# Performance work log

Measured on AMD Instinct MI355X. Metric: run time of the kernel, lower is better.

The kernel has to match this reference:

```python
import jax, jax.numpy as jnp
import numpy as np

B, LQ, LK = 16, 256, 256
DQ = DK = DV = H = 256


def setup_inputs() -> dict:
    key = jax.random.key(0)
    ks = jax.random.split(key, 7)
    queries = jax.random.normal(ks[0], (B, LQ, DQ), dtype=jnp.float32)
    keys = jax.random.normal(ks[1], (B, LK, DK), dtype=jnp.float32)
    values = jax.random.normal(ks[2], (B, LK, DV), dtype=jnp.float32)
    valid_lens = jax.random.randint(ks[3], (B,), 1, LK + 1).astype(jnp.int32)
    W_q = jax.random.normal(ks[4], (DQ, H), dtype=jnp.float32) / np.sqrt(DQ)
    W_k = jax.random.normal(ks[5], (DK, H), dtype=jnp.float32) / np.sqrt(DK)
    w_v = jax.random.normal(ks[6], (H,), dtype=jnp.float32) / np.sqrt(H)
    return {"queries": queries, "keys": keys, "values": values,
            "valid_lens": valid_lens, "W_q": W_q, "W_k": W_k, "w_v": w_v}


def reference(queries, keys, values, valid_lens, W_q, W_k, w_v):
    # Project queries and keys to the hidden size (no bias)
    q = jnp.einsum('bqd,dh->bqh', queries, W_q)          # (B, Lq, H)
    k = jnp.einsum('bkd,dh->bkh', keys, W_k)             # (B, Lk, H)
    # Broadcast-add, tanh, then contract with w_v -> scores (B, Lq, Lk)
    features = jnp.tanh(q[:, :, None, :] + k[:, None, :, :])  # (B, Lq, Lk, H)
    scores = jnp.einsum('bqkh,h->bqk', features, w_v)
    # Masked softmax over last axis: positions >= valid_len get -1e6
    mask = jnp.arange(scores.shape[-1]) < valid_lens[:, None, None]  # (B,1,Lk) bcast
    scores = jnp.where(mask, scores, jnp.float32(-1e6))
    attn = jax.nn.softmax(scores, axis=-1)
    # Dropout is identity at inference (training=False)
    return jnp.einsum('bqk,bkv->bqv', attn, values)      # (B, Lq, Dv)
```

## Files before the change

### kernel.cpp

```cpp
#include <hip/hip_runtime.h>

using bf16x8 = __attribute__((ext_vector_type(8))) __bf16;
using f32x4  = __attribute__((ext_vector_type(4))) float;
using f32x2  = __attribute__((ext_vector_type(2))) float;
using us8    = __attribute__((ext_vector_type(8))) unsigned short;

#define TWO_LOG2E 2.8853900817779268f
#define LOG2E 1.4426950408889634f

__device__ __forceinline__ unsigned short f2bf(float x) {
  unsigned int u = __float_as_uint(x);
  u = (u + 0x7fffu + ((u >> 16) & 1u)) >> 16;
  return (unsigned short)u;
}
__device__ __forceinline__ float bf2f(unsigned short h) {
  return __uint_as_float(((unsigned int)h) << 16);
}
__device__ __forceinline__ f32x2 pk_fma(f32x2 a, f32x2 b, f32x2 c) {
  return __builtin_elementwise_fma(a, b, c);
}

__global__ __launch_bounds__(256) void tcast_kernel(
    const float* __restrict__ Wq, const float* __restrict__ Wk,
    const float* __restrict__ vals, const float* __restrict__ wv,
    const int* __restrict__ vlens,
    unsigned short* __restrict__ wt_hi, unsigned short* __restrict__ wt_lo,
    unsigned short* __restrict__ vt_hi, unsigned short* __restrict__ vt_lo,
    float* __restrict__ wv2, float* __restrict__ Wsum,
    int* __restrict__ ctr, int* __restrict__ cum) {
  if (blockIdx.x == 0) {
    int t = threadIdx.x;
    wv2[t] = -2.0f * wv[t];
    if (t < 64) {
      float s = wv[t] + wv[t + 64] + wv[t + 128] + wv[t + 192];
#pragma unroll
      for (int off = 1; off < 64; off <<= 1) s += __shfl_xor(s, off, 64);
      if (t == 0) Wsum[0] = s;
    }
    if (t == 0) {
      ctr[0] = 0;
      int c = 0;
      for (int b = 0; b < 16; ++b) {
        cum[b] = c;
        c += ((vlens[b] + 31) >> 5) << 3;
      }
      cum[16] = c;
    }
  }
  __shared__ float tile[32][33];
  int m = blockIdx.x >> 6;
  int ts = blockIdx.x & 63;
  int R0 = (ts >> 3) << 5, C0 = (ts & 7) << 5;
  const float* src = (m == 0) ? Wq : (m == 1) ? Wk : (vals + ((m - 2) << 16));
  int r = threadIdx.x >> 3, c4 = (threadIdx.x & 7) << 2;
  float4 v = *(const float4*)(src + (R0 + r) * 256 + C0 + c4);
  tile[r][c4] = v.x; tile[r][c4 + 1] = v.y; tile[r][c4 + 2] = v.z; tile[r][c4 + 3] = v.w;
  __syncthreads();
  float o0 = tile[c4 + 0][r], o1 = tile[c4 + 1][r];
  float o2 = tile[c4 + 2][r], o3 = tile[c4 + 3][r];
  unsigned short h0 = f2bf(o0), h1 = f2bf(o1), h2 = f2bf(o2), h3 = f2bf(o3);
  int base = ((m < 2) ? (m << 16) : ((m - 2) << 16)) + (C0 + r) * 256 + R0 + c4;
  unsigned short* dh = (m < 2) ? wt_hi : vt_hi;
  unsigned short* dl = (m < 2) ? wt_lo : vt_lo;
  *(ushort4*)(dh + base) = make_ushort4(h0, h1, h2, h3);
  *(ushort4*)(dl + base) = make_ushort4(f2bf(o0 - bf2f(h0)), f2bf(o1 - bf2f(h1)),
                                        f2bf(o2 - bf2f(h2)), f2bf(o3 - bf2f(h3)));
}

__global__ __launch_bounds__(256, 4) void proj_kernel(
    const float* __restrict__ q, const float* __restrict__ kk,
    const unsigned short* __restrict__ w_hi, const unsigned short* __restrict__ w_lo,
    const int* __restrict__ vlens, float* __restrict__ Rq, float* __restrict__ RkT) {
  int wave = threadIdx.x >> 6, lane = threadIdx.x & 63;
  int mt = (blockIdx.x << 1) + (wave & 1);
  int m0 = mt << 4;
  int g = mt >> 8;
  if (g) {
    int bb = (m0 >> 8) & 15;
    if ((m0 & 255) >= vlens[bb]) return;
  }
  int r = lane & 15, qd = lane >> 4;
  int row = m0 + r;
  const float* A = (g == 0) ? (q + row * 256) : (kk + (row - 4096) * 256);
  bf16x8 ah[8], al[8];
#pragma unroll
  for (int s = 0; s < 8; ++s) {
    const float* p = A + qd * 8 + s * 32;
    float4 f0 = *(const float4*)p;
    float4 f1 = *(const float4*)(p + 4);
    float fv[8] = {f0.x, f0.y, f0.z, f0.w, f1.x, f1.y, f1.z, f1.w};
#pragma unroll
    for (int j = 0; j < 8; ++j) {
      __bf16 h = (__bf16)fv[j];
      ah[s][j] = h;
      al[s][j] = (__bf16)(fv[j] - (float)h);
    }
  }
  int nbase = (blockIdx.y << 6) + ((wave >> 1) << 5);
#pragma unroll
  for (int tI = 0; tI < 2; ++tI) {
    int n0 = nbase + (tI << 4);
    int boff = (g << 16) + (n0 + r) * 256 + qd * 8;
    f32x4 acc = {0.f, 0.f, 0.f, 0.f};
#pragma unroll
    for (int s = 0; s < 8; ++s) {
      bf16x8 bh = *(const bf16x8*)(w_hi + boff + s * 32);
      bf16x8 bl = *(const bf16x8*)(w_lo + boff + s * 32);
      acc = __builtin_amdgcn_mfma_f32_16x16x32_bf16(ah[s], bh, acc, 0, 0, 0);
      acc = __builtin_amdgcn_mfma_f32_16x16x32_bf16(ah[s], bl, acc, 0, 0, 0);
      acc = __builtin_amdgcn_mfma_f32_16x16x32_bf16(al[s], bh, acc, 0, 0, 0);
    }
    f32x4 ex;
#pragma unroll
    for (int i = 0; i < 4; ++i) {
      float l = acc[i] * TWO_LOG2E;
      l = fminf(fmaxf(l, -27.f), 27.f);
      ex[i] = __builtin_amdgcn_exp2f(l);
    }
    if (g == 0) {
#pragma unroll
      for (int i = 0; i < 4; ++i)
        Rq[(m0 + qd * 4 + i) * 256 + n0 + r] = ex[i];
    } else {
      int b = (m0 >> 8) & 15;
      int kloc = (m0 & 255) + qd * 4;
      *(f32x4*)(RkT + (b << 16) + (n0 + r) * 256 + kloc) = ex;
    }
  }
}

__global__ __launch_bounds__(256, 8) void scores_kernel(
    const float* __restrict__ Rq, const float* __restrict__ RkT,
    const float* __restrict__ wv2, const float* __restrict__ Wsum,
    const int* __restrict__ cum, int* __restrict__ ctr,
    float* __restrict__ sc) {
  __shared__ __align__(16) float rqs[32 * 76];
  __shared__ __align__(16) float kT[64 * 34];
  __shared__ int s_item;
  const int t = threadIdx.x;
  const int tq = t >> 4, tk = t & 15;
  const int sr = t >> 3, shb = (t & 7) << 3;
  const int hrow = t >> 2, kq = (t & 3) << 3;
  const int total = cum[16];
  const float ws = Wsum[0];

  for (;;) {
    __syncthreads();
    if (t == 0) s_item = atomicAdd(ctr, 1);
    __syncthreads();
    const int w = s_item;
    if (w >= total) return;
    int b = 0;
    while (cum[b + 1] <= w) ++b;
    const int local = w - cum[b];
    const int k0 = (local >> 3) << 5;
    const int q0 = (local & 7) << 5;
    const int qrow = (b << 8) + q0;
    f32x2 a0 = {0.f, 0.f}, a1 = {0.f, 0.f};

    for (int hc = 0; hc < 4; ++hc) {
      if (hc) __syncthreads();
      const float* gq = Rq + (qrow + sr) * 256 + (hc << 6) + shb;
      *(float4*)(rqs + sr * 76 + shb)     = *(const float4*)gq;
      *(float4*)(rqs + sr * 76 + shb + 4) = *(const float4*)(gq + 4);
      const float* gk = RkT + (b << 16) + ((hc << 6) + hrow) * 256 + k0 + kq;
      *(float4*)(kT + hrow * 34 + kq)     = *(const float4*)gk;
      *(float4*)(kT + hrow * 34 + kq + 4) = *(const float4*)(gk + 4);
      __syncthreads();
#pragma unroll 2
      for (int h = 0; h < 64; h += 4) {
        f32x4 qa = *(const f32x4*)(rqs + tq * 76 + h);
        f32x4 qb = *(const f32x4*)(rqs + (tq + 16) * 76 + h);
        f32x4 wm = *(const f32x4*)(wv2 + (hc << 6) + h);
#pragma unroll
        for (int j = 0; j < 4; ++j) {
          f32x2 rk = *(const f32x2*)(kT + (h + j) * 34 + (tk << 1));
          f32x2 wj = (f32x2)(wm[j]);
          f32x2 d0 = pk_fma(rk, (f32x2)(qa[j]), (f32x2)(1.0f));
          f32x2 d1 = pk_fma(rk, (f32x2)(qb[j]), (f32x2)(1.0f));
          f32x2 r0, r1;
          r0.x = __uint_as_float(0x7EF311C3u - __float_as_uint(d0.x));
          r0.y = __uint_as_float(0x7EF311C3u - __float_as_uint(d0.y));
          r1.x = __uint_as_float(0x7EF311C3u - __float_as_uint(d1.x));
          r1.y = __uint_as_float(0x7EF311C3u - __float_as_uint(d1.y));
          r0 = r0 * pk_fma(-d0, r0, (f32x2)(2.0f));
          r1 = r1 * pk_fma(-d1, r1, (f32x2)(2.0f));
          a0 = pk_fma(r0, wj, a0);
          a1 = pk_fma(r1, wj, a1);
        }
      }
    }
    a0 += (f32x2)(ws);
    a1 += (f32x2)(ws);
    *(f32x2*)(sc + ((qrow + tq) << 8) + k0 + (tk << 1)) = a0;
    *(f32x2*)(sc + ((qrow + tq + 16) << 8) + k0 + (tk << 1)) = a1;
  }
}

__global__ __launch_bounds__(256) void av_fused_kernel(
    const float* __restrict__ sc, const int* __restrict__ vlens,
    const unsigned short* __restrict__ vhi, const unsigned short* __restrict__ vlo,
    float* __restrict__ out) {
  __shared__ __align__(16) unsigned short athi[16 * 264];
  const int wave = threadIdx.x >> 6, lane = threadIdx.x & 63;
  const int b = blockIdx.x;
  const int nh = blockIdx.y;
  const int m0 = blockIdx.z << 4;
  const int vl = vlens[b];

  {
    int row = (wave << 2) + (lane & 3);
    int c0 = (lane >> 2) << 4;
    const float* srow = sc + ((b << 8) + m0 + row) * 256 + c0;
    float4 x0 = *(const float4*)(srow);
    float4 x1 = *(const float4*)(srow + 4);
    float4 x2 = *(const float4*)(srow + 8);
    float4 x3 = *(const float4*)(srow + 12);
    float p[16] = {x0.x, x0.y, x0.z, x0.w, x1.x, x1.y, x1.z, x1.w,
                   x2.x, x2.y, x2.z, x2.w, x3.x, x3.y, x3.z, x3.w};
#pragma unroll
    for (int i = 0; i < 16; ++i)
      if (c0 + i >= vl) p[i] = -1e6f;
    float mx = p[0];
#pragma unroll
    for (int i = 1; i < 16; ++i) mx = fmaxf(mx, p[i]);
#pragma unroll
    for (int off = 4; off <= 32; off <<= 1) mx = fmaxf(mx, __shfl_xor(mx, off, 64));
    float sm = 0.f;
#pragma unroll
    for (int i = 0; i < 16; ++i) {
      p[i] = __builtin_amdgcn_exp2f((p[i] - mx) * LOG2E);
      sm += p[i];
    }
#pragma unroll
    for (int off = 4; off <= 32; off <<= 1) sm += __shfl_xor(sm, off, 64);
    float rs = __builtin_amdgcn_rcpf(sm);
    us8 vh[2];
#pragma unroll
    for (int i = 0; i < 16; ++i) vh[i >> 3][i & 7] = f2bf(p[i] * rs);
    *(us8*)(athi + row * 264 + c0)     = vh[0];
    *(us8*)(athi + row * 264 + c0 + 8) = vh[1];
  }
  __syncthreads();

  const int r = lane & 15, qd = lane >> 4;
  const int smax = (vl + 31) >> 5;
#pragma unroll
  for (int tI = 0; tI < 2; ++tI) {
    int n0 = (nh << 7) + (wave << 5) + (tI << 4);
    int boff = (b << 16) + (n0 + r) * 256 + qd * 8;
    f32x4 acc = {0.f, 0.f, 0.f, 0.f};
    for (int s = 0; s < smax; ++s) {
      bf16x8 ah = *(const bf16x8*)(athi + r * 264 + qd * 8 + s * 32);
      bf16x8 bh = *(const bf16x8*)(vhi + boff + s * 32);
      bf16x8 bl = *(const bf16x8*)(vlo + boff + s * 32);
      acc = __builtin_amdgcn_mfma_f32_16x16x32_bf16(ah, bh, acc, 0, 0, 0);
      acc = __builtin_amdgcn_mfma_f32_16x16x32_bf16(ah, bl, acc, 0, 0, 0);
    }
#pragma unroll
    for (int i = 0; i < 4; ++i)
      out[(b << 16) + (m0 + qd * 4 + i) * 256 + n0 + r] = acc[i];
  }
}

extern "C" void kernel_launch(void* const* d_in, const int* in_sizes, int n_in,
                              void* d_out, int out_size, void* d_ws, size_t ws_size,
                              hipStream_t stream) {
  const float* queries = (const float*)d_in[0];
  const float* keys    = (const float*)d_in[1];
  const float* values  = (const float*)d_in[2];
  const int*   vlens   = (const int*)d_in[3];
  const float* Wq      = (const float*)d_in[4];
  const float* Wk      = (const float*)d_in[5];
  const float* wv      = (const float*)d_in[6];
  float* out = (float*)d_out;
  char* ws = (char*)d_ws;

  unsigned short* wt_hi = (unsigned short*)(ws + 0);
  unsigned short* wt_lo = (unsigned short*)(ws + 262144);
  unsigned short* vt_hi = (unsigned short*)(ws + 524288);
  unsigned short* vt_lo = (unsigned short*)(ws + 2621440);
  float*          Rq    = (float*)(ws + 4718592);
  float*          RkT   = (float*)(ws + 8912896);
  float*          sc    = (float*)(ws + 13107200);
  float*          wv2   = (float*)(ws + 17301504);
  float*          Wsum  = (float*)(ws + 17302528);
  int*            ctr   = (int*)(ws + 17302532);
  int*            cum   = (int*)(ws + 17302536);

  tcast_kernel<<<1152, 256, 0, stream>>>(Wq, Wk, values, wv, vlens,
                                         wt_hi, wt_lo, vt_hi, vt_lo, wv2, Wsum,
                                         ctr, cum);
  proj_kernel<<<dim3(256, 4), 256, 0, stream>>>(queries, keys, wt_hi, wt_lo,
                                                vlens, Rq, RkT);
  scores_kernel<<<512, 256, 0, stream>>>(Rq, RkT, wv2, Wsum, cum, ctr, sc);
  av_fused_kernel<<<dim3(16, 2, 16), 256, 0, stream>>>(sc, vlens, vt_hi, vt_lo, out);
}
```

Before: 135.3 us.

## Restructure proj and AV MFMA loops and relax scores launch bounds

The projection kernel now splits the K dimension into two halves and keeps both output tiles' accumulators live at once, which lowers register pressure from the bf16 hi/lo A fragments and interleaves the independent MFMA chains. The AV kernel drops the column-half grid dimension so each wave computes four 16-column tiles. This reuses the softmax probabilities across all 256 output columns and avoids recomputing the softmax in two blocks, at the cost of half as many blocks. The scores kernel's launch-bounds occupancy hint drops from 8 to 2, giving it more registers but possibly lower occupancy.

```diff
diff --git a/kernel.cpp b/kernel.cpp
--- a/kernel.cpp
+++ b/kernel.cpp
@@ -82,34 +82,45 @@
   int r = lane & 15, qd = lane >> 4;
   int row = m0 + r;
   const float* A = (g == 0) ? (q + row * 256) : (kk + (row - 4096) * 256);
-  bf16x8 ah[8], al[8];
-#pragma unroll
-  for (int s = 0; s < 8; ++s) {
-    const float* p = A + qd * 8 + s * 32;
-    float4 f0 = *(const float4*)p;
-    float4 f1 = *(const float4*)(p + 4);
-    float fv[8] = {f0.x, f0.y, f0.z, f0.w, f1.x, f1.y, f1.z, f1.w};
-#pragma unroll
-    for (int j = 0; j < 8; ++j) {
-      __bf16 h = (__bf16)fv[j];
-      ah[s][j] = h;
-      al[s][j] = (__bf16)(fv[j] - (float)h);
-    }
-  }
   int nbase = (blockIdx.y << 6) + ((wave >> 1) << 5);
+  int boff0 = (g << 16) + (nbase + r) * 256 + qd * 8;
+  int boff1 = boff0 + (16 << 8);
+  f32x4 acc0 = {0.f, 0.f, 0.f, 0.f}, acc1 = {0.f, 0.f, 0.f, 0.f};
+#pragma unroll
+  for (int kh = 0; kh < 2; ++kh) {
+    bf16x8 ah[4], al[4];
+#pragma unroll
+    for (int s = 0; s < 4; ++s) {
+      const float* p = A + qd * 8 + (kh * 4 + s) * 32;
+      float4 f0 = *(const float4*)p;
+      float4 f1 = *(const float4*)(p + 4);
+      float fv[8] = {f0.x, f0.y, f0.z, f0.w, f1.x, f1.y, f1.z, f1.w};
+#pragma unroll
+      for (int j = 0; j < 8; ++j) {
+        __bf16 h = (__bf16)fv[j];
+        ah[s][j] = h;
+        al[s][j] = (__bf16)(fv[j] - (float)h);
+      }
+    }
+#pragma unroll
+    for (int s = 0; s < 4; ++s) {
+      int off = (kh * 4 + s) * 32;
+      bf16x8 bh0 = *(const bf16x8*)(w_hi + boff0 + off);
+      bf16x8 bl0 = *(const bf16x8*)(w_lo + boff0 + off);
+      acc0 = __builtin_amdgcn_mfma_f32_16x16x32_bf16(ah[s], bh0, acc0, 0, 0, 0);
+      acc0 = __builtin_amdgcn_mfma_f32_16x16x32_bf16(ah[s], bl0, acc0, 0, 0, 0);
+      acc0 = __builtin_amdgcn_mfma_f32_16x16x32_bf16(al[s], bh0, acc0, 0, 0, 0);
+      bf16x8 bh1 = *(const bf16x8*)(w_hi + boff1 + off);
+      bf16x8 bl1 = *(const bf16x8*)(w_lo + boff1 + off);
+      acc1 = __builtin_amdgcn_mfma_f32_16x16x32_bf16(ah[s], bh1, acc1, 0, 0, 0);
+      acc1 = __builtin_amdgcn_mfma_f32_16x16x32_bf16(ah[s], bl1, acc1, 0, 0, 0);
+      acc1 = __builtin_amdgcn_mfma_f32_16x16x32_bf16(al[s], bh1, acc1, 0, 0, 0);
+    }
+  }
 #pragma unroll
   for (int tI = 0; tI < 2; ++tI) {
+    f32x4 acc = tI ? acc1 : acc0;
     int n0 = nbase + (tI << 4);
-    int boff = (g << 16) + (n0 + r) * 256 + qd * 8;
-    f32x4 acc = {0.f, 0.f, 0.f, 0.f};
-#pragma unroll
-    for (int s = 0; s < 8; ++s) {
-      bf16x8 bh = *(const bf16x8*)(w_hi + boff + s * 32);
-      bf16x8 bl = *(const bf16x8*)(w_lo + boff + s * 32);
-      acc = __builtin_amdgcn_mfma_f32_16x16x32_bf16(ah[s], bh, acc, 0, 0, 0);
-      acc = __builtin_amdgcn_mfma_f32_16x16x32_bf16(ah[s], bl, acc, 0, 0, 0);
-      acc = __builtin_amdgcn_mfma_f32_16x16x32_bf16(al[s], bh, acc, 0, 0, 0);
-    }
     f32x4 ex;
 #pragma unroll
     for (int i = 0; i < 4; ++i) {
@@ -129,7 +140,7 @@
   }
 }
 
-__global__ __launch_bounds__(256, 8) void scores_kernel(
+__global__ __launch_bounds__(256, 2) void scores_kernel(
     const float* __restrict__ Rq, const float* __restrict__ RkT,
     const float* __restrict__ wv2, const float* __restrict__ Wsum,
     const int* __restrict__ cum, int* __restrict__ ctr,
@@ -204,8 +215,7 @@
   __shared__ __align__(16) unsigned short athi[16 * 264];
   const int wave = threadIdx.x >> 6, lane = threadIdx.x & 63;
   const int b = blockIdx.x;
-  const int nh = blockIdx.y;
-  const int m0 = blockIdx.z << 4;
+  const int m0 = blockIdx.y << 4;
   const int vl = vlens[b];
 
   {
@@ -245,22 +255,25 @@
 
   const int r = lane & 15, qd = lane >> 4;
   const int smax = (vl + 31) >> 5;
-#pragma unroll
-  for (int tI = 0; tI < 2; ++tI) {
-    int n0 = (nh << 7) + (wave << 5) + (tI << 4);
-    int boff = (b << 16) + (n0 + r) * 256 + qd * 8;
-    f32x4 acc = {0.f, 0.f, 0.f, 0.f};
-    for (int s = 0; s < smax; ++s) {
-      bf16x8 ah = *(const bf16x8*)(athi + r * 264 + qd * 8 + s * 32);
-      bf16x8 bh = *(const bf16x8*)(vhi + boff + s * 32);
-      bf16x8 bl = *(const bf16x8*)(vlo + boff + s * 32);
-      acc = __builtin_amdgcn_mfma_f32_16x16x32_bf16(ah, bh, acc, 0, 0, 0);
-      acc = __builtin_amdgcn_mfma_f32_16x16x32_bf16(ah, bl, acc, 0, 0, 0);
-    }
+  const int nb = wave << 6;
+  const int boff = (b << 16) + (nb + r) * 256 + qd * 8;
+  f32x4 acc[4] = {{0.f,0.f,0.f,0.f},{0.f,0.f,0.f,0.f},
+                  {0.f,0.f,0.f,0.f},{0.f,0.f,0.f,0.f}};
+  for (int s = 0; s < smax; ++s) {
+    bf16x8 pa = *(const bf16x8*)(athi + r * 264 + qd * 8 + s * 32);
+#pragma unroll
+    for (int tI = 0; tI < 4; ++tI) {
+      bf16x8 bh = *(const bf16x8*)(vhi + boff + (tI << 12) + s * 32);
+      bf16x8 bl = *(const bf16x8*)(vlo + boff + (tI << 12) + s * 32);
+      acc[tI] = __builtin_amdgcn_mfma_f32_16x16x32_bf16(pa, bh, acc[tI], 0, 0, 0);
+      acc[tI] = __builtin_amdgcn_mfma_f32_16x16x32_bf16(pa, bl, acc[tI], 0, 0, 0);
+    }
+  }
+#pragma unroll
+  for (int tI = 0; tI < 4; ++tI)
 #pragma unroll
     for (int i = 0; i < 4; ++i)
-      out[(b << 16) + (m0 + qd * 4 + i) * 256 + n0 + r] = acc[i];
-  }
+      out[(b << 16) + (m0 + qd * 4 + i) * 256 + nb + (tI << 4) + r] = acc[tI][i];
 }
 
 extern "C" void kernel_launch(void* const* d_in, const int* in_sizes, int n_in,
@@ -294,5 +307,5 @@
   proj_kernel<<<dim3(256, 4), 256, 0, stream>>>(queries, keys, wt_hi, wt_lo,
                                                 vlens, Rq, RkT);
   scores_kernel<<<512, 256, 0, stream>>>(Rq, RkT, wv2, Wsum, cum, ctr, sc);
-  av_fused_kernel<<<dim3(16, 2, 16), 256, 0, stream>>>(sc, vlens, vt_hi, vt_lo, out);
-}
+  av_fused_kernel<<<dim3(16, 16), 256, 0, stream>>>(sc, vlens, vt_hi, vt_lo, out);
+}
```

New measurement: 134.3 us. No clear change (-0.7%).
